# Kernel optimization log

Measured on AMD Instinct MI355X. Metric: run time of the kernel, lower is better.

Reference implementation:

```python
import jax, jax.numpy as jnp
import numpy as np

QLEN, B, D, NH, DH, DI = 1024, 4, 1024, 16, 64, 4096
KLEN = QLEN
RLEN = QLEN + KLEN
EPS = 1e-12
SCALE = 1.0 / (DH ** 0.5)


def layer_norm(x, g, b):
    mu = jnp.mean(x, axis=-1, keepdims=True)
    var = jnp.mean(jnp.square(x - mu), axis=-1, keepdims=True)
    return (x - mu) * jax.lax.rsqrt(var + EPS) * g + b


def rel_shift(x, klen):
    # x: [qlen, rlen, b, n] -> [qlen, klen, b, n] via XLNet reshape trick
    q, r_, b, n = x.shape
    x = jnp.reshape(x, (r_, q, b, n))[1:]
    x = jnp.reshape(x, (q, r_ - 1, b, n))[:, :klen]
    return x


def setup_inputs() -> dict:
    key = jax.random.key(0)
    ks = jax.random.split(key, 16)
    std = 0.02
    h = jax.random.normal(ks[0], (QLEN, B, D), jnp.float32)
    r = jax.random.normal(ks[1], (RLEN, B, D), jnp.float32)
    # causal mask: 1 where key position j > query position i (disallowed)
    m = (jnp.arange(KLEN)[None, :] > jnp.arange(QLEN)[:, None]).astype(jnp.float32)
    attn_mask = jnp.broadcast_to(m[:, :, None, None], (QLEN, KLEN, B, 1))
    # segment matrix: one-hot of (seg_i != seg_j), shape [q, k, b, 2]
    seg_ids = jax.random.randint(ks[2], (QLEN, B), 0, 2)
    diff = (seg_ids[:, None, :] != seg_ids[None, :, :]).astype(jnp.int32)
    seg_mat = jax.nn.one_hot(diff, 2, dtype=jnp.float32)
    p = lambda k, shape: jax.random.normal(k, shape, jnp.float32) * std
    return {
        'h': h, 'r': r, 'attn_mask': attn_mask, 'seg_mat': seg_mat,
        'q_w': p(ks[3], (D, NH, DH)), 'k_w': p(ks[4], (D, NH, DH)),
        'v_w': p(ks[5], (D, NH, DH)), 'o_w': p(ks[6], (D, NH, DH)),
        'r_w': p(ks[7], (D, NH, DH)),
        'r_r_bias': jnp.zeros((NH, DH), jnp.float32),
        'r_s_bias': jnp.zeros((NH, DH), jnp.float32),
        'r_w_bias': jnp.zeros((NH, DH), jnp.float32),
        'seg_embed': p(ks[8], (2, NH, DH)),
        'ln1_g': jnp.ones((D,), jnp.float32), 'ln1_b': jnp.zeros((D,), jnp.float32),
        'ff_w1': p(ks[9], (D, DI)), 'ff_b1': jnp.zeros((DI,), jnp.float32),
        'ff_w2': p(ks[10], (DI, D)), 'ff_b2': jnp.zeros((D,), jnp.float32),
        'ln2_g': jnp.ones((D,), jnp.float32), 'ln2_b': jnp.zeros((D,), jnp.float32),
    }


def reference(h, r, attn_mask, seg_mat, q_w, k_w, v_w, o_w, r_w,
              r_r_bias, r_s_bias, r_w_bias, seg_embed,
              ln1_g, ln1_b, ff_w1, ff_b1, ff_w2, ff_b2, ln2_g, ln2_b):
    # projections (single-stream: g=None, mems=None => cat == h)
    q_head = jnp.einsum('ibh,hnd->ibnd', h, q_w)
    k_head = jnp.einsum('ibh,hnd->ibnd', h, k_w)
    v_head = jnp.einsum('ibh,hnd->ibnd', h, v_w)
    k_r = jnp.einsum('ibh,hnd->ibnd', r, r_w)
    # content + relative position + segment bias terms
    ac = jnp.einsum('ibnd,jbnd->ijbn', q_head + r_w_bias, k_head)
    bd = jnp.einsum('ibnd,jbnd->ijbn', q_head + r_r_bias, k_r)
    bd = rel_shift(bd, KLEN)
    ef = jnp.einsum('ibnd,snd->ibns', q_head + r_s_bias, seg_embed)
    ef = jnp.einsum('ijbs,ibns->ijbn', seg_mat, ef)
    attn_score = (ac + bd + ef) * SCALE - 1e30 * attn_mask
    attn_prob = jax.nn.softmax(attn_score, axis=1)
    attn_vec = jnp.einsum('ijbn,jbnd->ibnd', attn_prob, v_head)
    # post-attention
    attn_out = jnp.einsum('ibnd,hnd->ibh', attn_vec, o_w) + h
    out = layer_norm(attn_out, ln1_g, ln1_b)
    # feed-forward
    ff = jax.nn.gelu(jnp.einsum('ibh,hf->ibf', out, ff_w1) + ff_b1, approximate=False)
    ff = jnp.einsum('ibf,fh->ibh', ff, ff_w2) + ff_b2
    return layer_norm(ff + out, ln2_g, ln2_b)
```

## Files before the change

kernel.cpp:

```cpp
#include <hip/hip_runtime.h>
#include <hip/hip_bf16.h>

using bf16 = __hip_bfloat16;
typedef __attribute__((ext_vector_type(8))) short short8;
typedef __attribute__((ext_vector_type(4))) float floatx4;

#define QLEN 1024
#define KLEN 1024
#define RLEN 2048
#define RUSED 1152
#define BB   4
#define DMODEL 1024
#define NH   16
#define DH   64
#define DI   4096
#define ND   1024
#define QKVS 3072
#define SCALE 0.125f

__device__ inline void gl_lds16(const bf16* g, bf16* l) {
  __builtin_amdgcn_global_load_lds(
      (__attribute__((address_space(1))) void*)(g),
      (__attribute__((address_space(3))) void*)(l), 16, 0, 0);
}

__global__ __launch_bounds__(256) void cvt_all(
    const float* __restrict__ h, const float* __restrict__ r,
    const float* __restrict__ ow,
    bf16* __restrict__ hb, bf16* __restrict__ rb, bf16* __restrict__ wo)
{
  const int id = blockIdx.x;
  const float* src; bf16* dst; int off;
  if (id < 2048)      { src = h;  dst = hb; off = id * 2048; }
  else if (id < 4352) { src = r;  dst = rb; off = (id - 2048) * 2048; }
  else                { src = ow; dst = wo; off = (id - 4352) * 2048; }
  const int idx = off + threadIdx.x * 8;
  const float4 a = *reinterpret_cast<const float4*>(src + idx);
  const float4 b = *reinterpret_cast<const float4*>(src + idx + 4);
  bf16 o[8] = {__float2bfloat16(a.x), __float2bfloat16(a.y),
               __float2bfloat16(a.z), __float2bfloat16(a.w),
               __float2bfloat16(b.x), __float2bfloat16(b.y),
               __float2bfloat16(b.z), __float2bfloat16(b.w)};
  *reinterpret_cast<uint4*>(dst + idx) = *reinterpret_cast<uint4*>(o);
}

__device__ inline void tconv_tile(const float* __restrict__ src, bf16* __restrict__ dst,
                                  int R, int C, int bx, int by, int tid) {
  __shared__ float tile[32][33];
  const int r0 = by * 32, c0 = bx * 32;
  {
    const int tr = tid >> 3, tc = (tid & 7) * 4;
    const float4 f = *reinterpret_cast<const float4*>(src + (size_t)(r0 + tr) * C + c0 + tc);
    tile[tr][tc + 0] = f.x; tile[tr][tc + 1] = f.y;
    tile[tr][tc + 2] = f.z; tile[tr][tc + 3] = f.w;
  }
  __syncthreads();
  {
    const int oc = tid >> 3, orr = (tid & 7) * 4;
    bf16 o[4];
#pragma unroll
    for (int u = 0; u < 4; ++u) o[u] = __float2bfloat16(tile[orr + u][oc]);
    *reinterpret_cast<uint2*>(dst + (size_t)(c0 + oc) * R + r0 + orr) = *reinterpret_cast<uint2*>(o);
  }
}

__global__ __launch_bounds__(256) void tconv_all(
    const float* __restrict__ qw, const float* __restrict__ kw,
    const float* __restrict__ vw, const float* __restrict__ rw,
    const float* __restrict__ w1, const float* __restrict__ w2,
    bf16* __restrict__ wqkvt, bf16* __restrict__ wrt,
    bf16* __restrict__ w1t, bf16* __restrict__ w2t)
{
  const int id = blockIdx.x;
  const int tid = threadIdx.x;
  if (id < 4096) {
    const int part = id >> 10, local = id & 1023;
    const float* src = (part == 0) ? qw : (part == 1) ? kw : (part == 2) ? vw : rw;
    bf16* dst = (part < 3) ? (wqkvt + (size_t)part * ND * DMODEL) : wrt;
    tconv_tile(src, dst, DMODEL, ND, local & 31, local >> 5, tid);
  } else if (id < 8192) {
    const int local = id - 4096;
    tconv_tile(w1, w1t, DMODEL, DI, local & 127, local >> 7, tid);
  } else {
    const int local = id - 8192;
    tconv_tile(w2, w2t, DI, DMODEL, local & 31, local >> 5, tid);
  }
}

__global__ __launch_bounds__(256) void seg_extract(const float* __restrict__ seg,
                                                   float* __restrict__ dsb) {
  const int idx = blockIdx.x * 256 + threadIdx.x;
  const int i = idx >> 2, b = idx & 3;
  dsb[b * QLEN + i] = seg[(size_t)(i * KLEN * BB + b) * 2 + 1];
}

__global__ __launch_bounds__(256) void gemm_bt(
    const bf16* __restrict__ A, const bf16* __restrict__ Bt,
    int M, int N, int K, int Ktot, int lda, int ldb,
    const float* __restrict__ bias, const float* __restrict__ resid, int act_gelu,
    float* __restrict__ outf, bf16* __restrict__ outb, int pstride)
{
  __shared__ bf16 As[128][32];
  __shared__ bf16 Bs[128][32];

  const int tid = threadIdx.x;
  const int m0b = blockIdx.y * 128;
  const int n0b = blockIdx.x * 128;
  const int z = blockIdx.z;
  const int kbeg = z * K;
  const int kcnt = min(K, Ktot - kbeg);
  A  += (size_t)kbeg;
  Bt += (size_t)kbeg;
  float* of = outf ? (outf + (size_t)z * pstride) : outf;
  bf16*  ob = outb ? (outb + (size_t)z * pstride) : outb;

  const int wave = tid >> 6, lane = tid & 63;
  const int wm = (wave & 1) * 64, wn = (wave >> 1) * 64;
  const int fl = lane & 15, quad = lane >> 4;

  const int lr = lane >> 2;
  const int cg = (((lane & 3) ^ ((lr >> 1) & 3)) << 3);
  const bf16* ga0 = A  + (size_t)(m0b + wave * 32 + lr) * lda + cg;
  const bf16* ga1 = ga0 + (size_t)16 * lda;
  const bf16* gb0 = Bt + (size_t)(n0b + wave * 32 + lr) * ldb + cg;
  const bf16* gb1 = gb0 + (size_t)16 * ldb;
  bf16* la0 = &As[wave * 32 + lr][(lane & 3) * 8];
  bf16* la1 = &As[wave * 32 + 16 + lr][(lane & 3) * 8];
  bf16* lb0 = &Bs[wave * 32 + lr][(lane & 3) * 8];
  bf16* lb1 = &Bs[wave * 32 + 16 + lr][(lane & 3) * 8];

  const int rc = ((quad ^ ((fl >> 1) & 3)) << 3);

  floatx4 acc[4][4];
#pragma unroll
  for (int mi = 0; mi < 4; ++mi)
#pragma unroll
    for (int ni = 0; ni < 4; ++ni) acc[mi][ni] = (floatx4){0.f, 0.f, 0.f, 0.f};

  for (int k0 = 0; k0 < kcnt; k0 += 32) {
    __syncthreads();
    gl_lds16(ga0 + k0, la0);
    gl_lds16(ga1 + k0, la1);
    gl_lds16(gb0 + k0, lb0);
    gl_lds16(gb1 + k0, lb1);
    __syncthreads();

    short8 af[4], bfv[4];
#pragma unroll
    for (int mi = 0; mi < 4; ++mi)
      af[mi] = *reinterpret_cast<const short8*>(&As[wm + mi * 16 + fl][rc]);
#pragma unroll
    for (int ni = 0; ni < 4; ++ni)
      bfv[ni] = *reinterpret_cast<const short8*>(&Bs[wn + ni * 16 + fl][rc]);
#pragma unroll
    for (int mi = 0; mi < 4; ++mi)
#pragma unroll
      for (int ni = 0; ni < 4; ++ni)
        acc[mi][ni] = __builtin_amdgcn_mfma_f32_16x16x32_bf16(af[mi], bfv[ni], acc[mi][ni], 0, 0, 0);
  }

#pragma unroll
  for (int mi = 0; mi < 4; ++mi) {
#pragma unroll
    for (int r = 0; r < 4; ++r) {
      const int row = m0b + wm + mi * 16 + quad * 4 + r;
#pragma unroll
      for (int ni = 0; ni < 4; ++ni) {
        const int col = n0b + wn + ni * 16 + fl;
        float v = acc[mi][ni][r];
        if (bias) v += bias[col];
        if (act_gelu) v = 0.5f * v * (1.0f + erff(v * 0.70710678118654752f));
        const size_t base = (size_t)row * N + col;
        if (resid) v += resid[base];
        if (of) of[base] = v;
        if (ob) ob[base] = __float2bfloat16(v);
      }
    }
  }
}

__device__ __forceinline__ void stage_pair(const bf16* gA, const bf16* gB,
                                           int lda, int ldb, size_t ko,
                                           bf16* lA, bf16* lB) {
#pragma unroll
  for (int i = 0; i < 4; ++i) {
    gl_lds16(gA + (size_t)(i * 64) * lda + ko, lA + i * 4096);
    gl_lds16(gB + (size_t)(i * 64) * ldb + ko, lB + i * 4096);
  }
}

__global__ __launch_bounds__(512, 2) void gemm256(
    const bf16* __restrict__ A, const bf16* __restrict__ Bt,
    int M, int N, int K, int Ktot, int lda, int ldb,
    const float* __restrict__ bias, int act_gelu,
    bf16* __restrict__ outb, int pstride)
{
  __shared__ __attribute__((aligned(16))) bf16 As[2][256 * 64];
  __shared__ __attribute__((aligned(16))) bf16 Bs[2][256 * 64];

  const int tid = threadIdx.x;
  const int wave = tid >> 6, lane = tid & 63;

  const int gX = gridDim.x;
  const int nwg = gX * gridDim.y;
  int lin = blockIdx.y * gX + blockIdx.x;
  {
    const int q = nwg >> 3, r = nwg & 7;
    const int xcd = lin & 7, idx = lin >> 3;
    lin = (xcd < r ? xcd * (q + 1) : r * (q + 1) + (xcd - r) * q) + idx;
  }
  const int n0b = (lin % gX) << 8;
  const int m0b = (lin / gX) << 8;

  const int z = blockIdx.z;
  const int kbeg = z * K;
  const int nkt = min(K, Ktot - kbeg) >> 6;
  const bf16* Ab = A + (size_t)kbeg;
  const bf16* Bb = Bt + (size_t)kbeg;
  bf16* ob = outb + (size_t)z * pstride;

  const int srow = lane >> 3;
  const int scol = ((lane & 7) ^ srow) << 3;
  const bf16* gA = Ab + (size_t)(m0b + wave * 8 + srow) * lda + scol;
  const bf16* gB = Bb + (size_t)(n0b + wave * 8 + srow) * ldb + scol;
  const int lofs = wave * (8 * 64) + lane * 8;
  bf16* lA0 = &As[0][lofs]; bf16* lA1 = &As[1][lofs];
  bf16* lB0 = &Bs[0][lofs]; bf16* lB1 = &Bs[1][lofs];

  const int fl = lane & 15, quad = lane >> 4;
  const int wm = (wave >> 2) * 128;
  const int wn = (wave & 3) * 64;
  const int ch0 = (quad ^ (fl & 7)) << 3;

  floatx4 acc[8][4];
#pragma unroll
  for (int mi = 0; mi < 8; ++mi)
#pragma unroll
    for (int ni = 0; ni < 4; ++ni) acc[mi][ni] = (floatx4){0.f, 0.f, 0.f, 0.f};

  stage_pair(gA, gB, lda, ldb, 0, lA0, lB0);
  if (nkt > 1) stage_pair(gA, gB, lda, ldb, 64, lA1, lB1);

  for (int kt = 0; kt < nkt; ++kt) {
    if (kt + 1 < nkt) {
      asm volatile("s_waitcnt vmcnt(8)" ::: "memory");
    } else {
      asm volatile("s_waitcnt vmcnt(0)" ::: "memory");
    }
    __builtin_amdgcn_s_barrier();
    __builtin_amdgcn_sched_barrier(0);

    const bf16* as = (kt & 1) ? &As[1][0] : &As[0][0];
    const bf16* bs = (kt & 1) ? &Bs[1][0] : &Bs[0][0];
#pragma unroll
    for (int ks = 0; ks < 2; ++ks) {
      const int ch = ch0 ^ (ks << 5);
      short8 af[8], bv[4];
#pragma unroll
      for (int mi = 0; mi < 8; ++mi)
        af[mi] = *reinterpret_cast<const short8*>(&as[(wm + mi * 16 + fl) * 64 + ch]);
#pragma unroll
      for (int ni = 0; ni < 4; ++ni)
        bv[ni] = *reinterpret_cast<const short8*>(&bs[(wn + ni * 16 + fl) * 64 + ch]);
#pragma unroll
      for (int mi = 0; mi < 8; ++mi)
#pragma unroll
        for (int ni = 0; ni < 4; ++ni)
          acc[mi][ni] = __builtin_amdgcn_mfma_f32_16x16x32_bf16(af[mi], bv[ni], acc[mi][ni], 0, 0, 0);
    }
    __builtin_amdgcn_sched_barrier(0);
    __builtin_amdgcn_s_barrier();
    if (kt + 2 < nkt)
      stage_pair(gA, gB, lda, ldb, (size_t)(kt + 2) << 6,
                 (kt & 1) ? lA1 : lA0, (kt & 1) ? lB1 : lB0);
  }

#pragma unroll
  for (int mi = 0; mi < 8; ++mi) {
#pragma unroll
    for (int r = 0; r < 4; ++r) {
      const int row = m0b + wm + mi * 16 + quad * 4 + r;
#pragma unroll
      for (int ni = 0; ni < 4; ++ni) {
        const int col = n0b + wn + ni * 16 + fl;
        float v = acc[mi][ni][r];
        if (bias) v += bias[col];
        if (act_gelu) v = 0.5f * v * (1.0f + erff(v * 0.70710678118654752f));
        ob[(size_t)row * N + col] = __float2bfloat16(v);
      }
    }
  }
}

__global__ __launch_bounds__(256, 3) void attn_kernel(
    const bf16* __restrict__ qkv, const bf16* __restrict__ kr,
    const float* __restrict__ dsb, const float* __restrict__ seg_embed,
    const float* __restrict__ rwb, const float* __restrict__ rrb,
    const float* __restrict__ rsb,
    bf16* __restrict__ av_out)
{
  const int bx = blockIdx.x;
  const int n  = bx & 15;
  const int b  = (bx >> 4) & 3;
  const int it = 15 - (bx >> 6);
  const int i0 = it * 64;
  const int tid = threadIdx.x;

  const bf16* qh = qkv + n * DH;
  const bf16* kh = qkv + ND + n * DH;
  const bf16* vh = qkv + 2 * ND + n * DH;

  __shared__ bf16 Kb[64][72];
  __shared__ bf16 VT[64][72];
  __shared__ bf16 krw[128][72];
  __shared__ bf16 bdrL[64][88];
  __shared__ float efs0[64], efs1[64];
  __shared__ float dsq[64], dsk[64];

  const int wave = tid >> 6, lane = tid & 63;
  const int fl = lane & 15, quad = lane >> 4;
  const int wq0 = wave * 16;
  const int tb0 = 3 - wave;
  const int twoc = (tid & 3) << 1;

  short8 aw[2], ar[2];
  {
    const int qrow = i0 + wq0 + fl;
    const bf16* qp = qh + (size_t)(qrow * BB + b) * QKVS;
    float e0 = 0.f, e1 = 0.f;
#pragma unroll
    for (int ks = 0; ks < 2; ++ks) {
      const int d0 = ks * 32 + quad * 8;
      const uint4 qv = *reinterpret_cast<const uint4*>(qp + d0);
      const bf16* qe = reinterpret_cast<const bf16*>(&qv);
      bf16 wt[8], rt[8];
#pragma unroll
      for (int u = 0; u < 8; ++u) {
        const int d = d0 + u;
        const float qf = __bfloat162float(qe[u]);
        wt[u] = __float2bfloat16(qf + rwb[n * DH + d]);
        rt[u] = __float2bfloat16(qf + rrb[n * DH + d]);
        const float qs = qf + rsb[n * DH + d];
        e0 += qs * seg_embed[(0 * NH + n) * DH + d];
        e1 += qs * seg_embed[(1 * NH + n) * DH + d];
      }
      aw[ks] = *reinterpret_cast<short8*>(wt);
      ar[ks] = *reinterpret_cast<short8*>(rt);
    }
    e0 += __shfl_xor(e0, 16, 64); e0 += __shfl_xor(e0, 32, 64);
    e1 += __shfl_xor(e1, 16, 64); e1 += __shfl_xor(e1, 32, 64);
    if (quad == 0) { efs0[wq0 + fl] = e0; efs1[wq0 + fl] = e1; }
    if (tid < 64) dsq[tid] = dsb[b * QLEN + i0 + tid];
  }

  floatx4 O[4];
#pragma unroll
  for (int nb = 0; nb < 4; ++nb) O[nb] = (floatx4){0.f, 0.f, 0.f, 0.f};
  float l_loc[4] = {0.f, 0.f, 0.f, 0.f};

  for (int jt = 0; jt <= it; ++jt) {
    const int j0 = jt * 64;
    const int kbase = QLEN + j0 - i0 - 63;

    __syncthreads();

    {
      const int j  = tid >> 2;
      const int dc = (tid & 3) << 4;
      const bf16* kp = kh + (size_t)((j0 + j) * BB + b) * QKVS + dc;
      const uint4 k0v = reinterpret_cast<const uint4*>(kp)[0];
      const uint4 k1v = reinterpret_cast<const uint4*>(kp)[1];
      reinterpret_cast<uint4*>(&Kb[j][dc])[0] = k0v;
      reinterpret_cast<uint4*>(&Kb[j][dc + 8])[0] = k1v;
      const bf16* vp = vh + (size_t)((j0 + j) * BB + b) * QKVS + dc;
      const uint4 v0v = reinterpret_cast<const uint4*>(vp)[0];
      const uint4 v1v = reinterpret_cast<const uint4*>(vp)[1];
      const bf16* ve0 = reinterpret_cast<const bf16*>(&v0v);
      const bf16* ve1 = reinterpret_cast<const bf16*>(&v1v);
#pragma unroll
      for (int u = 0; u < 8; ++u) {
        VT[dc + (u ^ twoc)][j] = ve0[u];
        VT[dc + 8 + (u ^ twoc)][j] = ve1[u];
      }
      const int t   = tid >> 1;
      const int dc2 = (tid & 1) << 5;
      const bf16* rp = kr + ((size_t)((kbase + t) * BB + b)) * ND + n * DH + dc2;
#pragma unroll
      for (int u = 0; u < 4; ++u)
        reinterpret_cast<uint4*>(&krw[t][dc2 + u * 8])[0] = reinterpret_cast<const uint4*>(rp)[u];
      if (tid < 64) dsk[tid] = dsb[b * QLEN + j0 + tid];
    }
    __syncthreads();

    floatx4 accS[4], accB[5];
#pragma unroll
    for (int nb = 0; nb < 4; ++nb) accS[nb] = (floatx4){0.f, 0.f, 0.f, 0.f};
#pragma unroll
    for (int u = 0; u < 5; ++u) accB[u] = (floatx4){0.f, 0.f, 0.f, 0.f};
#pragma unroll
    for (int ks = 0; ks < 2; ++ks) {
#pragma unroll
      for (int nb = 0; nb < 4; ++nb)
        accS[nb] = __builtin_amdgcn_mfma_f32_16x16x32_bf16(
            aw[ks], *reinterpret_cast<const short8*>(&Kb[nb * 16 + fl][ks * 32 + quad * 8]), accS[nb], 0, 0, 0);
#pragma unroll
      for (int u = 0; u < 5; ++u)
        accB[u] = __builtin_amdgcn_mfma_f32_16x16x32_bf16(
            ar[ks], *reinterpret_cast<const short8*>(&krw[(tb0 + u) * 16 + fl][ks * 32 + quad * 8]), accB[u], 0, 0, 0);
    }
#pragma unroll
    for (int u = 0; u < 5; ++u)
#pragma unroll
      for (int r = 0; r < 4; ++r)
        bdrL[wq0 + quad * 4 + r][u * 16 + fl] = __float2bfloat16(accB[u][r]);

    float pv[4][4];
#pragma unroll
    for (int r = 0; r < 4; ++r) {
      const int qL = wq0 + quad * 4 + r;
      const int qg = i0 + qL;
      const float e0q = efs0[qL], e1q = efs1[qL];
      const float dq = dsq[qL];
#pragma unroll
      for (int nb = 0; nb < 4; ++nb) {
        const int kL = nb * 16 + fl;
        const int kg = j0 + kL;
        const float bdv = __bfloat162float(bdrL[qL][15 + kL - quad * 4 - r]);
        const float ef = (dq != dsk[kL]) ? e1q : e0q;
        const float s = (accS[nb][r] + bdv + ef) * SCALE;
        const float pe = (kg > qg) ? 0.0f : __expf(s);
        pv[nb][r] = pe;
        l_loc[r] += pe;
      }
    }

#pragma unroll
    for (int nb = 0; nb < 4; ++nb)
#pragma unroll
      for (int r = 0; r < 4; ++r)
        bdrL[wq0 + quad * 4 + r][nb * 16 + fl] = __float2bfloat16(pv[nb][r]);

#pragma unroll
    for (int ks = 0; ks < 2; ++ks) {
      const short8 ap = *reinterpret_cast<const short8*>(&bdrL[wq0 + fl][ks * 32 + quad * 8]);
#pragma unroll
      for (int nb = 0; nb < 4; ++nb)
        O[nb] = __builtin_amdgcn_mfma_f32_16x16x32_bf16(
            ap, *reinterpret_cast<const short8*>(&VT[nb * 16 + (fl ^ (nb << 1))][ks * 32 + quad * 8]), O[nb], 0, 0, 0);
    }
  }

  float inv[4];
#pragma unroll
  for (int r = 0; r < 4; ++r) {
    float l = l_loc[r];
    l += __shfl_xor(l, 1, 64);
    l += __shfl_xor(l, 2, 64);
    l += __shfl_xor(l, 4, 64);
    l += __shfl_xor(l, 8, 64);
    inv[r] = 1.0f / l;
  }
#pragma unroll
  for (int r = 0; r < 4; ++r) {
    const int qL = wq0 + quad * 4 + r;
    bf16* op = av_out + ((size_t)((i0 + qL) * BB + b)) * ND + n * DH;
#pragma unroll
    for (int nb = 0; nb < 4; ++nb)
      op[nb * 16 + fl] = __float2bfloat16(O[nb][r] * inv[r]);
  }
}

__global__ __launch_bounds__(256) void ln_fused(
    const float* __restrict__ pa, const float* __restrict__ pb,
    const float* __restrict__ resid,
    const float* __restrict__ gg, const float* __restrict__ bbias,
    float* __restrict__ outf, bf16* __restrict__ outb)
{
  const int row = blockIdx.x;
  const int tid = threadIdx.x;
  __shared__ float red[4];
  const size_t base = (size_t)row * DMODEL;

  float v[4];
  float s = 0.0f;
#pragma unroll
  for (int k = 0; k < 4; ++k) {
    const int c = k * 256 + tid;
    const float x = pa[base + c] + pb[base + c] + resid[base + c];
    v[k] = x;
    s += x;
  }
#pragma unroll
  for (int off = 32; off; off >>= 1) s += __shfl_xor(s, off, 64);
  const int w = tid >> 6, lane = tid & 63;
  if (lane == 0) red[w] = s;
  __syncthreads();
  const float mean = (red[0] + red[1] + red[2] + red[3]) * (1.0f / DMODEL);

  float s2 = 0.0f;
#pragma unroll
  for (int k = 0; k < 4; ++k) {
    const float dlt = v[k] - mean;
    s2 += dlt * dlt;
  }
  __syncthreads();
#pragma unroll
  for (int off = 32; off; off >>= 1) s2 += __shfl_xor(s2, off, 64);
  if (lane == 0) red[w] = s2;
  __syncthreads();
  const float var = (red[0] + red[1] + red[2] + red[3]) * (1.0f / DMODEL);
  const float rstd = rsqrtf(var + 1e-12f);

#pragma unroll
  for (int k = 0; k < 4; ++k) {
    const int c = k * 256 + tid;
    const float o = (v[k] - mean) * rstd * gg[c] + bbias[c];
    if (outf) outf[base + c] = o;
    if (outb) outb[base + c] = __float2bfloat16(o);
  }
}

__global__ __launch_bounds__(256) void ln_fused4b(
    const bf16* __restrict__ pa, const bf16* __restrict__ pb,
    const bf16* __restrict__ pc, const bf16* __restrict__ pd,
    const float* __restrict__ resid, const float* __restrict__ bias,
    const float* __restrict__ gg, const float* __restrict__ bbias,
    float* __restrict__ outf)
{
  const int row = blockIdx.x;
  const int tid = threadIdx.x;
  __shared__ float red[4];
  const size_t base = (size_t)row * DMODEL;

  float v[4];
  float s = 0.0f;
#pragma unroll
  for (int k = 0; k < 4; ++k) {
    const int c = k * 256 + tid;
    float x = __bfloat162float(pa[base + c]) + __bfloat162float(pb[base + c]) +
              __bfloat162float(pc[base + c]) + __bfloat162float(pd[base + c]) +
              resid[base + c] + bias[c];
    v[k] = x;
    s += x;
  }
#pragma unroll
  for (int off = 32; off; off >>= 1) s += __shfl_xor(s, off, 64);
  const int w = tid >> 6, lane = tid & 63;
  if (lane == 0) red[w] = s;
  __syncthreads();
  const float mean = (red[0] + red[1] + red[2] + red[3]) * (1.0f / DMODEL);

  float s2 = 0.0f;
#pragma unroll
  for (int k = 0; k < 4; ++k) {
    const float dlt = v[k] - mean;
    s2 += dlt * dlt;
  }
  __syncthreads();
#pragma unroll
  for (int off = 32; off; off >>= 1) s2 += __shfl_xor(s2, off, 64);
  if (lane == 0) red[w] = s2;
  __syncthreads();
  const float var = (red[0] + red[1] + red[2] + red[3]) * (1.0f / DMODEL);
  const float rstd = rsqrtf(var + 1e-12f);

#pragma unroll
  for (int k = 0; k < 4; ++k) {
    const int c = k * 256 + tid;
    outf[base + c] = (v[k] - mean) * rstd * gg[c] + bbias[c];
  }
}

extern "C" void kernel_launch(void* const* d_in, const int* in_sizes, int n_in,
                              void* d_out, int out_size, void* d_ws, size_t ws_size,
                              hipStream_t stream) {
  const float* h         = (const float*)d_in[0];
  const float* r         = (const float*)d_in[1];
  const float* seg_mat   = (const float*)d_in[3];
  const float* q_w       = (const float*)d_in[4];
  const float* k_w       = (const float*)d_in[5];
  const float* v_w       = (const float*)d_in[6];
  const float* o_w       = (const float*)d_in[7];
  const float* r_w       = (const float*)d_in[8];
  const float* r_r_bias  = (const float*)d_in[9];
  const float* r_s_bias  = (const float*)d_in[10];
  const float* r_w_bias  = (const float*)d_in[11];
  const float* seg_embed = (const float*)d_in[12];
  const float* ln1_g     = (const float*)d_in[13];
  const float* ln1_b     = (const float*)d_in[14];
  const float* ff_w1     = (const float*)d_in[15];
  const float* ff_b1     = (const float*)d_in[16];
  const float* ff_w2     = (const float*)d_in[17];
  const float* ff_b2     = (const float*)d_in[18];
  const float* ln2_g     = (const float*)d_in[19];
  const float* ln2_b     = (const float*)d_in[20];
  float* outp = (float*)d_out;

  const size_t M1 = (size_t)QLEN * BB;
  const size_t MRU = (size_t)RUSED * BB;
  char* ws = (char*)d_ws;
  const size_t MB = 1u << 20;

  bf16* hb   = (bf16*)(ws + 0 * MB);
  bf16* rb   = (bf16*)(ws + 8 * MB);
  bf16* wqkvt= (bf16*)(ws + 24 * MB);
  bf16* wrt  = (bf16*)(ws + 30 * MB);
  bf16* wo   = (bf16*)(ws + 32 * MB);
  bf16* w1t  = (bf16*)(ws + 34 * MB);
  bf16* w2t  = (bf16*)(ws + 42 * MB);
  bf16* qkvb = (bf16*)(ws + 50 * MB);
  bf16* krb  = (bf16*)(ws + 74 * MB);
  bf16* avb  = (bf16*)(ws + 90 * MB);
  float* pa1  = (float*)(ws + 0 * MB);
  float* pb1  = (float*)(ws + 16 * MB);
  float* out1 = (float*)(ws + 50 * MB);
  bf16* out1b = (bf16*)(ws + 66 * MB);
  bf16* ff1   = (bf16*)(ws + 0 * MB);
  bf16* p2    = (bf16*)(ws + 74 * MB);
  float* dsbuf = (float*)(ws + 106 * MB);

  dim3 blk(256);
  dim3 blk512(512);

  cvt_all<<<dim3(4864), blk, 0, stream>>>(h, r, o_w, hb, rb, wo);
  tconv_all<<<dim3(12288), blk, 0, stream>>>(q_w, k_w, v_w, r_w, ff_w1, ff_w2,
                                             wqkvt, wrt, w1t, w2t);
  seg_extract<<<dim3(16), blk, 0, stream>>>(seg_mat, dsbuf);

  gemm256<<<dim3(QKVS / 256, M1 / 256, 1), blk512, 0, stream>>>(
      hb, wqkvt, (int)M1, QKVS, DMODEL, DMODEL, DMODEL, DMODEL, nullptr, 0, qkvb, 0);
  gemm_bt<<<dim3(ND / 128, (int)(MRU / 128), 1), blk, 0, stream>>>(
      rb, wrt, (int)MRU, ND, DMODEL, DMODEL, DMODEL, DMODEL, nullptr, nullptr, 0, nullptr, krb, 0);

  attn_kernel<<<dim3(16 * BB * NH), blk, 0, stream>>>(
      qkvb, krb, dsbuf, seg_embed,
      r_w_bias, r_r_bias, r_s_bias, avb);

  gemm_bt<<<dim3(DMODEL / 128, M1 / 128, 2), blk, 0, stream>>>(
      avb, wo, (int)M1, DMODEL, ND / 2, ND, ND, ND, nullptr, nullptr, 0, pa1, nullptr, (int)(M1 * DMODEL));

  ln_fused<<<dim3((int)M1), blk, 0, stream>>>(pa1, pb1, h, ln1_g, ln1_b, out1, out1b);

  gemm256<<<dim3(DI / 256, M1 / 256, 1), blk512, 0, stream>>>(
      out1b, w1t, (int)M1, DI, DMODEL, DMODEL, DMODEL, DMODEL, ff_b1, 1, ff1, 0);

  gemm256<<<dim3(DMODEL / 256, M1 / 256, 4), blk512, 0, stream>>>(
      ff1, w2t, (int)M1, DMODEL, DI / 4, DI, DI, DI, nullptr, 0, p2, (int)(M1 * DMODEL));

  ln_fused4b<<<dim3((int)M1), blk, 0, stream>>>(
      p2, p2 + M1 * DMODEL, p2 + 2 * M1 * DMODEL, p2 + 3 * M1 * DMODEL,
      out1, ff_b2, ln2_g, ln2_b, outp);
}
```

Baseline: 477.9 us.

## Shrink gemm256 tile to 256x128 with K-step 32 for higher occupancy

```diff
diff --git a/kernel.cpp b/kernel.cpp
--- a/kernel.cpp
+++ b/kernel.cpp
@@ -179,24 +179,14 @@
   }
 }
 
-__device__ __forceinline__ void stage_pair(const bf16* gA, const bf16* gB,
-                                           int lda, int ldb, size_t ko,
-                                           bf16* lA, bf16* lB) {
-#pragma unroll
-  for (int i = 0; i < 4; ++i) {
-    gl_lds16(gA + (size_t)(i * 64) * lda + ko, lA + i * 4096);
-    gl_lds16(gB + (size_t)(i * 64) * ldb + ko, lB + i * 4096);
-  }
-}
-
-__global__ __launch_bounds__(512, 2) void gemm256(
+__global__ __launch_bounds__(512, 6) void gemm256(
     const bf16* __restrict__ A, const bf16* __restrict__ Bt,
     int M, int N, int K, int Ktot, int lda, int ldb,
     const float* __restrict__ bias, int act_gelu,
     bf16* __restrict__ outb, int pstride)
 {
-  __shared__ __attribute__((aligned(16))) bf16 As[2][256 * 64];
-  __shared__ __attribute__((aligned(16))) bf16 Bs[2][256 * 64];
+  __shared__ __attribute__((aligned(16))) bf16 As[2][256 * 32];
+  __shared__ __attribute__((aligned(16))) bf16 Bs[2][128 * 32];
 
   const int tid = threadIdx.x;
   const int wave = tid >> 6, lane = tid & 63;
@@ -209,41 +199,49 @@
     const int xcd = lin & 7, idx = lin >> 3;
     lin = (xcd < r ? xcd * (q + 1) : r * (q + 1) + (xcd - r) * q) + idx;
   }
-  const int n0b = (lin % gX) << 8;
+  const int n0b = (lin % gX) << 7;
   const int m0b = (lin / gX) << 8;
 
   const int z = blockIdx.z;
   const int kbeg = z * K;
-  const int nkt = min(K, Ktot - kbeg) >> 6;
+  const int nkt = min(K, Ktot - kbeg) >> 5;
   const bf16* Ab = A + (size_t)kbeg;
   const bf16* Bb = Bt + (size_t)kbeg;
   bf16* ob = outb + (size_t)z * pstride;
 
-  const int srow = lane >> 3;
-  const int scol = ((lane & 7) ^ srow) << 3;
-  const bf16* gA = Ab + (size_t)(m0b + wave * 8 + srow) * lda + scol;
-  const bf16* gB = Bb + (size_t)(n0b + wave * 8 + srow) * ldb + scol;
-  const int lofs = wave * (8 * 64) + lane * 8;
-  bf16* lA0 = &As[0][lofs]; bf16* lA1 = &As[1][lofs];
-  bf16* lB0 = &Bs[0][lofs]; bf16* lB1 = &Bs[1][lofs];
+  const int srow = tid >> 2;
+  const int scol = (((tid & 3) ^ (srow & 3)) << 3);
+  const bf16* gA0 = Ab + (size_t)(m0b + srow) * lda + scol;
+  const bf16* gA1 = gA0 + (size_t)128 * lda;
+  const bf16* gB  = Bb + (size_t)(n0b + srow) * ldb + scol;
+  bf16* lA[2] = {&As[0][tid * 8], &As[1][tid * 8]};
+  bf16* lB[2] = {&Bs[0][tid * 8], &Bs[1][tid * 8]};
 
   const int fl = lane & 15, quad = lane >> 4;
-  const int wm = (wave >> 2) * 128;
-  const int wn = (wave & 3) * 64;
-  const int ch0 = (quad ^ (fl & 7)) << 3;
-
-  floatx4 acc[8][4];
-#pragma unroll
-  for (int mi = 0; mi < 8; ++mi)
+  const int wm = (wave >> 1) * 64;
+  const int wn = (wave & 1) * 64;
+  const int rch = ((quad ^ (fl & 3)) << 3);
+
+  floatx4 acc[4][4];
+#pragma unroll
+  for (int mi = 0; mi < 4; ++mi)
 #pragma unroll
     for (int ni = 0; ni < 4; ++ni) acc[mi][ni] = (floatx4){0.f, 0.f, 0.f, 0.f};
 
-  stage_pair(gA, gB, lda, ldb, 0, lA0, lB0);
-  if (nkt > 1) stage_pair(gA, gB, lda, ldb, 64, lA1, lB1);
+  {
+    gl_lds16(gA0, lA[0]);
+    gl_lds16(gA1, lA[0] + 4096);
+    gl_lds16(gB,  lB[0]);
+  }
+  if (nkt > 1) {
+    gl_lds16(gA0 + 32, lA[1]);
+    gl_lds16(gA1 + 32, lA[1] + 4096);
+    gl_lds16(gB  + 32, lB[1]);
+  }
 
   for (int kt = 0; kt < nkt; ++kt) {
     if (kt + 1 < nkt) {
-      asm volatile("s_waitcnt vmcnt(8)" ::: "memory");
+      asm volatile("s_waitcnt vmcnt(3)" ::: "memory");
     } else {
       asm volatile("s_waitcnt vmcnt(0)" ::: "memory");
     }
@@ -252,31 +250,34 @@
 
     const bf16* as = (kt & 1) ? &As[1][0] : &As[0][0];
     const bf16* bs = (kt & 1) ? &Bs[1][0] : &Bs[0][0];
-#pragma unroll
-    for (int ks = 0; ks < 2; ++ks) {
-      const int ch = ch0 ^ (ks << 5);
-      short8 af[8], bv[4];
-#pragma unroll
-      for (int mi = 0; mi < 8; ++mi)
-        af[mi] = *reinterpret_cast<const short8*>(&as[(wm + mi * 16 + fl) * 64 + ch]);
+    short8 af[4], bv[4];
+#pragma unroll
+    for (int mi = 0; mi < 4; ++mi)
+      af[mi] = *reinterpret_cast<const short8*>(&as[(wm + mi * 16 + fl) * 32 + rch]);
+#pragma unroll
+    for (int ni = 0; ni < 4; ++ni)
+      bv[ni] = *reinterpret_cast<const short8*>(&bs[(wn + ni * 16 + fl) * 32 + rch]);
+    __builtin_amdgcn_s_setprio(1);
+#pragma unroll
+    for (int mi = 0; mi < 4; ++mi)
 #pragma unroll
       for (int ni = 0; ni < 4; ++ni)
-        bv[ni] = *reinterpret_cast<const short8*>(&bs[(wn + ni * 16 + fl) * 64 + ch]);
-#pragma unroll
-      for (int mi = 0; mi < 8; ++mi)
-#pragma unroll
-        for (int ni = 0; ni < 4; ++ni)
-          acc[mi][ni] = __builtin_amdgcn_mfma_f32_16x16x32_bf16(af[mi], bv[ni], acc[mi][ni], 0, 0, 0);
-    }
+        acc[mi][ni] = __builtin_amdgcn_mfma_f32_16x16x32_bf16(af[mi], bv[ni], acc[mi][ni], 0, 0, 0);
+    __builtin_amdgcn_s_setprio(0);
     __builtin_amdgcn_sched_barrier(0);
     __builtin_amdgcn_s_barrier();
-    if (kt + 2 < nkt)
-      stage_pair(gA, gB, lda, ldb, (size_t)(kt + 2) << 6,
-                 (kt & 1) ? lA1 : lA0, (kt & 1) ? lB1 : lB0);
-  }
-
-#pragma unroll
-  for (int mi = 0; mi < 8; ++mi) {
+    if (kt + 2 < nkt) {
+      const int ko = (kt + 2) << 5;
+      bf16* dA = (kt & 1) ? lA[1] : lA[0];
+      bf16* dB = (kt & 1) ? lB[1] : lB[0];
+      gl_lds16(gA0 + ko, dA);
+      gl_lds16(gA1 + ko, dA + 4096);
+      gl_lds16(gB  + ko, dB);
+    }
+  }
+
+#pragma unroll
+  for (int mi = 0; mi < 4; ++mi) {
 #pragma unroll
     for (int r = 0; r < 4; ++r) {
       const int row = m0b + wm + mi * 16 + quad * 4 + r;
@@ -627,7 +628,7 @@
                                              wqkvt, wrt, w1t, w2t);
   seg_extract<<<dim3(16), blk, 0, stream>>>(seg_mat, dsbuf);
 
-  gemm256<<<dim3(QKVS / 256, M1 / 256, 1), blk512, 0, stream>>>(
+  gemm256<<<dim3(QKVS / 128, M1 / 256, 1), blk512, 0, stream>>>(
       hb, wqkvt, (int)M1, QKVS, DMODEL, DMODEL, DMODEL, DMODEL, nullptr, 0, qkvb, 0);
   gemm_bt<<<dim3(ND / 128, (int)(MRU / 128), 1), blk, 0, stream>>>(
       rb, wrt, (int)MRU, ND, DMODEL, DMODEL, DMODEL, DMODEL, nullptr, nullptr, 0, nullptr, krb, 0);
@@ -641,10 +642,10 @@
 
   ln_fused<<<dim3((int)M1), blk, 0, stream>>>(pa1, pb1, h, ln1_g, ln1_b, out1, out1b);
 
-  gemm256<<<dim3(DI / 256, M1 / 256, 1), blk512, 0, stream>>>(
+  gemm256<<<dim3(DI / 128, M1 / 256, 1), blk512, 0, stream>>>(
       out1b, w1t, (int)M1, DI, DMODEL, DMODEL, DMODEL, DMODEL, ff_b1, 1, ff1, 0);
 
-  gemm256<<<dim3(DMODEL / 256, M1 / 256, 4), blk512, 0, stream>>>(
+  gemm256<<<dim3(DMODEL / 128, M1 / 256, 4), blk512, 0, stream>>>(
       ff1, w2t, (int)M1, DMODEL, DI / 4, DI, DI, DI, nullptr, 0, p2, (int)(M1 * DMODEL));
 
   ln_fused4b<<<dim3((int)M1), blk, 0, stream>>>(
```

Result: slower. 1.155 ms (+141.7%).
